# Performance work log

Hardware: AMD Instinct MI355X
Metric: run time of the kernel (lower is better)

Reference implementation:

```python
import jax, jax.numpy as jnp
import numpy as np

WINDOW_PAD = 2
OUT_NUM = 5

def setup_inputs() -> dict:
    key = jax.random.key(0)
    ks = jax.random.split(key, 7)
    B, T, E, V, H = 64, 512, 300, 50000, 2048
    in_feat = (2 * WINDOW_PAD + 1) * E + OUT_NUM * WINDOW_PAD  # 1510
    return {
        "idxs": jax.random.randint(ks[0], (B, T), 0, V),
        "emb_table": jax.random.normal(ks[1], (V, E), dtype=jnp.float32),
        "W1": jax.random.normal(ks[2], (in_feat, H), dtype=jnp.float32) * 0.02,
        "b1": jax.random.normal(ks[3], (H,), dtype=jnp.float32) * 0.02,
        "W2": jax.random.normal(ks[4], (H, OUT_NUM), dtype=jnp.float32) * 0.02,
        "b2": jax.random.normal(ks[5], (OUT_NUM,), dtype=jnp.float32) * 0.02,
        "initial_state": jnp.zeros((OUT_NUM * WINDOW_PAD,), dtype=jnp.float32),
    }

def reference(idxs, emb_table, W1, b1, W2, b2, initial_state):
    B, T = idxs.shape
    E = emb_table.shape[1]
    wp = WINDOW_PAD
    # pad token indices with 0 on both sides, gather embeddings
    idxs_pad = jnp.pad(idxs, ((0, 0), (wp, wp)))          # [B, T+2wp]
    emb_pad = emb_table[idxs_pad]                          # [B, T+2wp, E]
    # sliding windows: position t sees tokens t..t+2wp of padded seq
    win = jnp.stack([emb_pad[:, k:k + T, :] for k in range(2 * wp + 1)], axis=2)
    e = win.reshape(B, T, (2 * wp + 1) * E)                # [B, T, (2wp+1)E]
    e_t = jnp.transpose(e, (1, 0, 2))                      # [T, B, F] for scan

    prev0 = jnp.tile(initial_state[None, :], (B, 1))       # [B, out*wp]

    def step(prev, e_i):
        x_i = jnp.concatenate([e_i, prev], axis=1)         # [B, F + out*wp]
        h = jax.nn.relu(x_i @ W1 + b1)                     # [B, H]
        y_i = h @ W2 + b2                                  # [B, out]
        p = jax.nn.softmax(jax.lax.stop_gradient(y_i), axis=1)
        new_prev = jnp.concatenate([prev[:, OUT_NUM:], p], axis=1)
        return new_prev, y_i

    _, ys = jax.lax.scan(step, prev0, e_t)                 # ys: [T, B, out]
    return jnp.transpose(ys, (1, 0, 2))                    # [B, T, out]
```

## Files before the change

kernel.cpp:

```cpp
#include <hip/hip_runtime.h>

typedef __attribute__((ext_vector_type(8))) short bf16x8;
typedef __attribute__((ext_vector_type(8))) unsigned short u16x8;
typedef __attribute__((ext_vector_type(4))) float f32x4;
typedef __attribute__((ext_vector_type(2))) float f32x2;

__device__ __forceinline__ unsigned short f2bf(float f) {
  union { float f; unsigned u; } v; v.f = f;
  unsigned r = v.u + 0x7FFFu + ((v.u >> 16) & 1u);
  return (unsigned short)(r >> 16);
}
__device__ __forceinline__ float bf2f(unsigned short s) {
  union { unsigned u; float f; } v; v.u = ((unsigned)s) << 16;
  return v.f;
}
__device__ __forceinline__ float max3f(float a, float b, float c) {
  float d;
  asm("v_max3_f32 %0, %1, %2, %3" : "=v"(d) : "v"(a), "v"(b), "v"(c));
  return d;
}

template <int CTRL>
__device__ __forceinline__ float dpp_add(float v) {
  int m = __builtin_amdgcn_update_dpp(0, __float_as_int(v), CTRL, 0xf, 0xf, true);
  return v + __int_as_float(m);
}
__device__ __forceinline__ float wave_sum63(float v) {
  v = dpp_add<0x111>(v);
  v = dpp_add<0x112>(v);
  v = dpp_add<0x114>(v);
  v = dpp_add<0x118>(v);
  v = dpp_add<0x142>(v);
  v = dpp_add<0x143>(v);
  return v;
}


__global__ __launch_bounds__(256) void prep_kernel(
    const float* __restrict__ W1, unsigned short* __restrict__ W1bT,
    const int* __restrict__ idxs, const float* __restrict__ emb,
    unsigned short* __restrict__ P) {
  const int bid = blockIdx.x;
  const int tid = threadIdx.x;
  if (bid < 800) {
    __shared__ float tile[64][65];
    int kb = bid % 25;
    int hb = bid / 25;
    int win = kb / 5;
    int e0 = (kb % 5) << 6;
    int hh = tid & 63;
    int kq = tid >> 6;
#pragma unroll
    for (int kk = kq; kk < 64; kk += 4) {
      int e = e0 + kk;
      float v = 0.f;
      if (e < 300) v = W1[(size_t)(win * 300 + e) * 2048 + hb * 64 + hh];
      tile[kk][hh] = v;
    }
    __syncthreads();
    int kk = tid & 63;
    int hq = tid >> 6;
#pragma unroll
    for (int h = hq; h < 64; h += 4) {
      W1bT[(size_t)(hb * 64 + h) * 1600 + kb * 64 + kk] = f2bf(tile[kk][h]);
    }
    return;
  }
  int g4 = (bid - 800) * 4;
#pragma unroll
  for (int r = 0; r < 4; ++r) {
    int g = g4 + r;
    int b = g / 516;
    int tp = g - b * 516;
    int tok = 0;
    if (tp >= 2 && tp < 514) tok = idxs[b * 512 + tp - 2];
    const float* erow = emb + (size_t)tok * 300;
    float v = (tid < 300) ? erow[tid] : 0.f;
    P[(size_t)g * 320 + tid] = f2bf(v);
    if (tid < 64) {
      int e = tid + 256;
      float v2 = (e < 300) ? erow[e] : 0.f;
      P[(size_t)g * 320 + e] = f2bf(v2);
    }
  }
}

__global__ __launch_bounds__(256) void gemm_kernel(
    const unsigned short* __restrict__ P,
    const unsigned short* __restrict__ W1bT,
    const float* __restrict__ b1,
    unsigned short* __restrict__ Z) {
  __shared__ unsigned short smem[17408];
  unsigned short* As = smem;
  unsigned short* Bs = smem + 8192;
  const int tid = threadIdx.x;
  const int lane = tid & 63;
  const int w = tid >> 6;
  const int wm = w >> 1, wn = w & 1;
  const int lr = lane & 15;
  const int lk = (lane >> 4) << 3;

  const int nt = blockIdx.x & 15;
  const int mt = blockIdx.x >> 4;
  const int b = mt >> 2;
  const int t0 = (mt & 3) << 7;

  const unsigned short* srcA[4];
  const unsigned short* srcB[4];
#pragma unroll
  for (int j = 0; j < 4; ++j) {
    int chunk = tid + j * 256;
    int row = chunk >> 3, kb = chunk & 7;
    int kbs = kb ^ (row & 7);
    srcA[j] = P + (size_t)(b * 516 + t0 + row) * 320 + (kbs << 3);
    srcB[j] = W1bT + (size_t)(nt * 128 + row) * 1600 + (kbs << 3);
  }

  f32x4 acc[4][4];
#pragma unroll
  for (int i = 0; i < 4; i++)
#pragma unroll
    for (int j = 0; j < 4; j++) acc[i][j] = (f32x4){0.f, 0.f, 0.f, 0.f};

  for (int kt = 0; kt < 25; ++kt) {
#pragma unroll
    for (int j = 0; j < 4; ++j) {
      int chunk = tid + j * 256;
      __builtin_amdgcn_global_load_lds(
          (const __attribute__((address_space(1))) unsigned int*)srcA[j],
          (__attribute__((address_space(3))) unsigned int*)&As[chunk << 3],
          16, 0, 0);
      srcA[j] += 64;
    }
#pragma unroll
    for (int j = 0; j < 4; ++j) {
      int chunk = tid + j * 256;
      __builtin_amdgcn_global_load_lds(
          (const __attribute__((address_space(1))) unsigned int*)srcB[j],
          (__attribute__((address_space(3))) unsigned int*)&Bs[chunk << 3],
          16, 0, 0);
      srcB[j] += 64;
    }
    __syncthreads();
#pragma unroll
    for (int ks = 0; ks < 64; ks += 32) {
      const int slot = (ks + lk) >> 3;
      bf16x8 af[4], bv[4];
#pragma unroll
      for (int am = 0; am < 4; ++am) {
        int row = (wm << 6) + (am << 4) + lr;
        af[am] = *(const bf16x8*)&As[(row << 6) + ((slot ^ (row & 7)) << 3)];
      }
#pragma unroll
      for (int bn = 0; bn < 4; ++bn) {
        int col = (wn << 6) + (bn << 4) + lr;
        bv[bn] = *(const bf16x8*)&Bs[(col << 6) + ((slot ^ (col & 7)) << 3)];
      }
#pragma unroll
      for (int am = 0; am < 4; ++am)
#pragma unroll
        for (int bn = 0; bn < 4; ++bn)
          acc[am][bn] = __builtin_amdgcn_mfma_f32_16x16x32_bf16(
              af[am], bv[bn], acc[am][bn], 0, 0, 0);
    }
    __syncthreads();
  }

  {
    const int rq = lane >> 4;
    const int rloc0 = (wm << 6) + (rq << 2);
    const int cloc0 = (wn << 6) + lr;
    float b1v[4];
#pragma unroll
    for (int bn = 0; bn < 4; ++bn)
      b1v[bn] = b1[nt * 128 + cloc0 + (bn << 4)];
#pragma unroll
    for (int am = 0; am < 4; ++am)
#pragma unroll
      for (int bn = 0; bn < 4; ++bn) {
        int rl = rloc0 + (am << 4);
        int cl = cloc0 + (bn << 4);
#pragma unroll
        for (int j = 0; j < 4; ++j)
          smem[(rl + j) * 136 + cl] = f2bf(acc[am][bn][j] + b1v[bn]);
      }
    __syncthreads();
    const int chunk = tid & 15;
    const int rsub = tid >> 4;
#pragma unroll
    for (int p = 0; p < 8; ++p) {
      int row = p * 16 + rsub;
      u16x8 v = *(const u16x8*)&smem[row * 136 + chunk * 8];
      *(u16x8*)&Z[(size_t)(mt * 128 + row) * 2048 + nt * 128 + chunk * 8] = v;
    }
  }
}

__global__ __launch_bounds__(256, 1) void scan_kernel(
    const unsigned short* __restrict__ Z, const float* __restrict__ W1,
    const float* __restrict__ W2, const float* __restrict__ b2,
    const float* __restrict__ istate, float* __restrict__ out) {
  const int b = blockIdx.x;
  const int tid = threadIdx.x;
  const int lane = tid & 63;
  const int wv = tid >> 6;
  const unsigned short* Zb = Z + (size_t)b * 512 * 2048;
  float* outb = out + (size_t)b * 512 * 5;

  f32x2 w1p[4][10];
#pragma unroll
  for (int i = 0; i < 10; ++i) {
    const float* row = &W1[(size_t)(1500 + i) * 2048 + tid * 8];
#pragma unroll
    for (int q = 0; q < 4; ++q) w1p[q][i] = *(const f32x2*)&row[q * 2];
  }
  f32x2 w2p[4][5];
#pragma unroll
  for (int k = 0; k < 5; ++k)
#pragma unroll
    for (int q = 0; q < 4; ++q)
      w2p[q][k] = (f32x2){W2[(tid * 8 + 2 * q) * 5 + k],
                          W2[(tid * 8 + 2 * q + 1) * 5 + k]};
  const float b20 = b2[0], b21 = b2[1], b22 = b2[2], b23 = b2[3],
              b24 = b2[4];
  const float L2E = 1.4426950408889634f;

  __shared__ float part[2][4][8];
  __shared__ float out_lds[512][8];

  float ef0 = istate[5], ef1 = istate[6], ef2 = istate[7], ef3 = istate[8],
        ef4 = istate[9];
  float rf = 1.0f;

  u16x8 zc0 = *(const u16x8*)&Zb[tid * 8];
  u16x8 zn = *(const u16x8*)&Zb[(size_t)2048 + tid * 8];
  u16x8 zf = *(const u16x8*)&Zb[(size_t)2 * 2048 + tid * 8];
  f32x2 xc[4];
  xc[0] = (f32x2){bf2f(zc0[0]), bf2f(zc0[1])};
  xc[1] = (f32x2){bf2f(zc0[2]), bf2f(zc0[3])};
  xc[2] = (f32x2){bf2f(zc0[4]), bf2f(zc0[5])};
  xc[3] = (f32x2){bf2f(zc0[6]), bf2f(zc0[7])};
#pragma unroll
  for (int i = 0; i < 5; ++i) {
    const float oi = istate[i];
#pragma unroll
    for (int q = 0; q < 4; ++q) xc[q] = oi * w1p[q][i] + xc[q];
  }

  for (int t = 0; t < 512; ++t) {
    f32x2 sA0 = ef0 * w1p[0][5], sA1 = ef0 * w1p[1][5],
          sA2 = ef0 * w1p[2][5], sA3 = ef0 * w1p[3][5];
    sA0 = ef1 * w1p[0][6] + sA0; sA1 = ef1 * w1p[1][6] + sA1;
    sA2 = ef1 * w1p[2][6] + sA2; sA3 = ef1 * w1p[3][6] + sA3;
    sA0 = ef2 * w1p[0][7] + sA0; sA1 = ef2 * w1p[1][7] + sA1;
    sA2 = ef2 * w1p[2][7] + sA2; sA3 = ef2 * w1p[3][7] + sA3;
    sA0 = ef3 * w1p[0][8] + sA0; sA1 = ef3 * w1p[1][8] + sA1;
    sA2 = ef3 * w1p[2][8] + sA2; sA3 = ef3 * w1p[3][8] + sA3;
    sA0 = ef4 * w1p[0][9] + sA0; sA1 = ef4 * w1p[1][9] + sA1;
    sA2 = ef4 * w1p[2][9] + sA2; sA3 = ef4 * w1p[3][9] + sA3;
    f32x2 x0 = rf * sA0 + xc[0];
    f32x2 x1 = rf * sA1 + xc[1];
    f32x2 x2 = rf * sA2 + xc[2];
    f32x2 x3 = rf * sA3 + xc[3];
    const f32x2 zero2 = (f32x2){0.f, 0.f};
    x0 = __builtin_elementwise_max(x0, zero2);
    x1 = __builtin_elementwise_max(x1, zero2);
    x2 = __builtin_elementwise_max(x2, zero2);
    x3 = __builtin_elementwise_max(x3, zero2);
    f32x2 a0 = x0 * w2p[0][0] + x1 * w2p[1][0];
    f32x2 a1 = x0 * w2p[0][1] + x1 * w2p[1][1];
    f32x2 a2 = x0 * w2p[0][2] + x1 * w2p[1][2];
    f32x2 a3 = x0 * w2p[0][3] + x1 * w2p[1][3];
    f32x2 a4 = x0 * w2p[0][4] + x1 * w2p[1][4];
    a0 = x2 * w2p[2][0] + a0;  a0 = x3 * w2p[3][0] + a0;
    a1 = x2 * w2p[2][1] + a1;  a1 = x3 * w2p[3][1] + a1;
    a2 = x2 * w2p[2][2] + a2;  a2 = x3 * w2p[3][2] + a2;
    a3 = x2 * w2p[2][3] + a3;  a3 = x3 * w2p[3][3] + a3;
    a4 = x2 * w2p[2][4] + a4;  a4 = x3 * w2p[3][4] + a4;
    float y0 = a0.x + a0.y, y1 = a1.x + a1.y, y2 = a2.x + a2.y,
          y3 = a3.x + a3.y, y4 = a4.x + a4.y;

    int tn = (t + 3 < 512) ? (t + 3) : 511;
    u16x8 zfn = *(const u16x8*)&Zb[(size_t)tn * 2048 + tid * 8];

    y0 = wave_sum63(y0);
    y1 = wave_sum63(y1);
    y2 = wave_sum63(y2);
    y3 = wave_sum63(y3);
    y4 = wave_sum63(y4);
    const int pp = t & 1;
    if (lane == 63) {
      *(float4*)&part[pp][wv][0] = (float4){y0, y1, y2, y3};
      part[pp][wv][4] = y4;
    }
    asm volatile("s_waitcnt lgkmcnt(0)" ::: "memory");
    __builtin_amdgcn_sched_barrier(0);
    __builtin_amdgcn_s_barrier();
    __builtin_amdgcn_sched_barrier(0);

    f32x4 q0 = *(const f32x4*)&part[pp][0][0];
    f32x4 q1 = *(const f32x4*)&part[pp][1][0];
    f32x4 q2 = *(const f32x4*)&part[pp][2][0];
    f32x4 q3 = *(const f32x4*)&part[pp][3][0];
    f32x4 sv = (q0 + q1) + (q2 + q3);
    float s4 = (part[pp][0][4] + part[pp][1][4]) +
               (part[pp][2][4] + part[pp][3][4]);
    float s0 = sv.x + b20, s1 = sv.y + b21, s2 = sv.z + b22,
          s3 = sv.w + b23;
    s4 += b24;

    f32x2 xe0 = ef0 * w1p[0][0], xe1 = ef0 * w1p[1][0],
          xe2 = ef0 * w1p[2][0], xe3 = ef0 * w1p[3][0];
    xe0 = ef1 * w1p[0][1] + xe0; xe1 = ef1 * w1p[1][1] + xe1;
    xe2 = ef1 * w1p[2][1] + xe2; xe3 = ef1 * w1p[3][1] + xe3;
    xe0 = ef2 * w1p[0][2] + xe0; xe1 = ef2 * w1p[1][2] + xe1;
    xe2 = ef2 * w1p[2][2] + xe2; xe3 = ef2 * w1p[3][2] + xe3;
    xe0 = ef3 * w1p[0][3] + xe0; xe1 = ef3 * w1p[1][3] + xe1;
    xe2 = ef3 * w1p[2][3] + xe2; xe3 = ef3 * w1p[3][3] + xe3;
    xe0 = ef4 * w1p[0][4] + xe0; xe1 = ef4 * w1p[1][4] + xe1;
    xe2 = ef4 * w1p[2][4] + xe2; xe3 = ef4 * w1p[3][4] + xe3;
    f32x2 zn0 = (f32x2){bf2f(zn[0]), bf2f(zn[1])};
    f32x2 zn1 = (f32x2){bf2f(zn[2]), bf2f(zn[3])};
    f32x2 zn2 = (f32x2){bf2f(zn[4]), bf2f(zn[5])};
    f32x2 zn3 = (f32x2){bf2f(zn[6]), bf2f(zn[7])};
    xc[0] = rf * xe0 + zn0;
    xc[1] = rf * xe1 + zn1;
    xc[2] = rf * xe2 + zn2;
    xc[3] = rf * xe3 + zn3;

    if (tid == 0) {
      *(float4*)&out_lds[t][0] = (float4){s0, s1, s2, s3};
      out_lds[t][4] = s4;
    }

    float m = max3f(s0, s1, s2);
    m = max3f(m, s3, s4);
    float mL = m * L2E;
    ef0 = __builtin_amdgcn_exp2f(fmaf(s0, L2E, -mL));
    ef1 = __builtin_amdgcn_exp2f(fmaf(s1, L2E, -mL));
    ef2 = __builtin_amdgcn_exp2f(fmaf(s2, L2E, -mL));
    ef3 = __builtin_amdgcn_exp2f(fmaf(s3, L2E, -mL));
    ef4 = __builtin_amdgcn_exp2f(fmaf(s4, L2E, -mL));
    float d = ((ef0 + ef1) + (ef2 + ef3)) + ef4;
    rf = __builtin_amdgcn_rcpf(d);

    zn = zf; zf = zfn;
  }

  __syncthreads();
  {
    const int r0 = tid * 2, r1 = tid * 2 + 1;
    float o[10];
#pragma unroll
    for (int i = 0; i < 5; ++i) o[i] = out_lds[r0][i];
#pragma unroll
    for (int i = 0; i < 5; ++i) o[5 + i] = out_lds[r1][i];
    float* dst = outb + tid * 10;
#pragma unroll
    for (int i = 0; i < 10; ++i) dst[i] = o[i];
  }
}

extern "C" void kernel_launch(void* const* d_in, const int* in_sizes, int n_in,
                              void* d_out, int out_size, void* d_ws,
                              size_t ws_size, hipStream_t stream) {
  const int* idxs = (const int*)d_in[0];
  const float* emb = (const float*)d_in[1];
  const float* W1 = (const float*)d_in[2];
  const float* b1 = (const float*)d_in[3];
  const float* W2 = (const float*)d_in[4];
  const float* b2 = (const float*)d_in[5];
  const float* istate = (const float*)d_in[6];
  float* out = (float*)d_out;

  char* ws = (char*)d_ws;
  unsigned short* P = (unsigned short*)ws;
  unsigned short* W1bT = (unsigned short*)(ws + 21135360);
  unsigned short* Z = (unsigned short*)(ws + 21135360 + 6553600);

  hipLaunchKernelGGL(prep_kernel, dim3(800 + 8256), dim3(256), 0, stream,
                     W1, W1bT, idxs, emb, P);
  hipLaunchKernelGGL(gemm_kernel, dim3(256 * 16), dim3(256), 0, stream, P, W1bT, b1, Z);
  hipLaunchKernelGGL(scan_kernel, dim3(64), dim3(256), 0, stream, Z, W1, W2, b2,
                     istate, out);
}
```

Before: 532.6 us.

## Halve scan block to 128 threads with 16 hidden units per thread

The sequential scan kernel now uses 2 waves instead of 4, and each thread handles 16 hidden units instead of 8, so the per-step cross-wave reduction reads 2 partials instead of 4. The goal is a shorter per-timestep critical path through the barrier and LDS reduction. In exchange each thread does twice the FMA work per step and holds twice as many weights in registers, which lengthens the serial arithmetic chain and raises register pressure.

Measured after the change: 629.5 us. 1.18x slower.

```diff
diff --git a/kernel.cpp b/kernel.cpp
--- a/kernel.cpp
+++ b/kernel.cpp
@@ -196,7 +196,7 @@
   }
 }
 
-__global__ __launch_bounds__(256, 1) void scan_kernel(
+__global__ __launch_bounds__(128, 1) void scan_kernel(
     const unsigned short* __restrict__ Z, const float* __restrict__ W1,
     const float* __restrict__ W2, const float* __restrict__ b2,
     const float* __restrict__ istate, float* __restrict__ out) {
@@ -207,81 +207,80 @@
   const unsigned short* Zb = Z + (size_t)b * 512 * 2048;
   float* outb = out + (size_t)b * 512 * 5;
 
-  f32x2 w1p[4][10];
+  f32x2 w1p[8][10];
 #pragma unroll
   for (int i = 0; i < 10; ++i) {
-    const float* row = &W1[(size_t)(1500 + i) * 2048 + tid * 8];
-#pragma unroll
-    for (int q = 0; q < 4; ++q) w1p[q][i] = *(const f32x2*)&row[q * 2];
-  }
-  f32x2 w2p[4][5];
+    const float* row = &W1[(size_t)(1500 + i) * 2048 + tid * 16];
+#pragma unroll
+    for (int q = 0; q < 8; ++q) w1p[q][i] = *(const f32x2*)&row[q * 2];
+  }
+  f32x2 w2p[8][5];
 #pragma unroll
   for (int k = 0; k < 5; ++k)
 #pragma unroll
-    for (int q = 0; q < 4; ++q)
-      w2p[q][k] = (f32x2){W2[(tid * 8 + 2 * q) * 5 + k],
-                          W2[(tid * 8 + 2 * q + 1) * 5 + k]};
+    for (int q = 0; q < 8; ++q)
+      w2p[q][k] = (f32x2){W2[(tid * 16 + 2 * q) * 5 + k],
+                          W2[(tid * 16 + 2 * q + 1) * 5 + k]};
   const float b20 = b2[0], b21 = b2[1], b22 = b2[2], b23 = b2[3],
               b24 = b2[4];
   const float L2E = 1.4426950408889634f;
 
-  __shared__ float part[2][4][8];
+  __shared__ float part[2][2][8];
   __shared__ float out_lds[512][8];
 
   float ef0 = istate[5], ef1 = istate[6], ef2 = istate[7], ef3 = istate[8],
         ef4 = istate[9];
   float rf = 1.0f;
 
-  u16x8 zc0 = *(const u16x8*)&Zb[tid * 8];
-  u16x8 zn = *(const u16x8*)&Zb[(size_t)2048 + tid * 8];
-  u16x8 zf = *(const u16x8*)&Zb[(size_t)2 * 2048 + tid * 8];
-  f32x2 xc[4];
-  xc[0] = (f32x2){bf2f(zc0[0]), bf2f(zc0[1])};
-  xc[1] = (f32x2){bf2f(zc0[2]), bf2f(zc0[3])};
-  xc[2] = (f32x2){bf2f(zc0[4]), bf2f(zc0[5])};
-  xc[3] = (f32x2){bf2f(zc0[6]), bf2f(zc0[7])};
+  u16x8 zcA = *(const u16x8*)&Zb[tid * 16];
+  u16x8 zcB = *(const u16x8*)&Zb[tid * 16 + 8];
+  u16x8 znA = *(const u16x8*)&Zb[(size_t)2048 + tid * 16];
+  u16x8 znB = *(const u16x8*)&Zb[(size_t)2048 + tid * 16 + 8];
+  u16x8 zfA = *(const u16x8*)&Zb[(size_t)2 * 2048 + tid * 16];
+  u16x8 zfB = *(const u16x8*)&Zb[(size_t)2 * 2048 + tid * 16 + 8];
+
+  f32x2 xc[8];
+#pragma unroll
+  for (int q = 0; q < 4; ++q) {
+    xc[q] = (f32x2){bf2f(zcA[2 * q]), bf2f(zcA[2 * q + 1])};
+    xc[4 + q] = (f32x2){bf2f(zcB[2 * q]), bf2f(zcB[2 * q + 1])};
+  }
 #pragma unroll
   for (int i = 0; i < 5; ++i) {
     const float oi = istate[i];
 #pragma unroll
-    for (int q = 0; q < 4; ++q) xc[q] = oi * w1p[q][i] + xc[q];
+    for (int q = 0; q < 8; ++q) xc[q] = oi * w1p[q][i] + xc[q];
   }
 
   for (int t = 0; t < 512; ++t) {
-    f32x2 sA0 = ef0 * w1p[0][5], sA1 = ef0 * w1p[1][5],
-          sA2 = ef0 * w1p[2][5], sA3 = ef0 * w1p[3][5];
-    sA0 = ef1 * w1p[0][6] + sA0; sA1 = ef1 * w1p[1][6] + sA1;
-    sA2 = ef1 * w1p[2][6] + sA2; sA3 = ef1 * w1p[3][6] + sA3;
-    sA0 = ef2 * w1p[0][7] + sA0; sA1 = ef2 * w1p[1][7] + sA1;
-    sA2 = ef2 * w1p[2][7] + sA2; sA3 = ef2 * w1p[3][7] + sA3;
-    sA0 = ef3 * w1p[0][8] + sA0; sA1 = ef3 * w1p[1][8] + sA1;
-    sA2 = ef3 * w1p[2][8] + sA2; sA3 = ef3 * w1p[3][8] + sA3;
-    sA0 = ef4 * w1p[0][9] + sA0; sA1 = ef4 * w1p[1][9] + sA1;
-    sA2 = ef4 * w1p[2][9] + sA2; sA3 = ef4 * w1p[3][9] + sA3;
-    f32x2 x0 = rf * sA0 + xc[0];
-    f32x2 x1 = rf * sA1 + xc[1];
-    f32x2 x2 = rf * sA2 + xc[2];
-    f32x2 x3 = rf * sA3 + xc[3];
-    const f32x2 zero2 = (f32x2){0.f, 0.f};
-    x0 = __builtin_elementwise_max(x0, zero2);
-    x1 = __builtin_elementwise_max(x1, zero2);
-    x2 = __builtin_elementwise_max(x2, zero2);
-    x3 = __builtin_elementwise_max(x3, zero2);
-    f32x2 a0 = x0 * w2p[0][0] + x1 * w2p[1][0];
-    f32x2 a1 = x0 * w2p[0][1] + x1 * w2p[1][1];
-    f32x2 a2 = x0 * w2p[0][2] + x1 * w2p[1][2];
-    f32x2 a3 = x0 * w2p[0][3] + x1 * w2p[1][3];
-    f32x2 a4 = x0 * w2p[0][4] + x1 * w2p[1][4];
-    a0 = x2 * w2p[2][0] + a0;  a0 = x3 * w2p[3][0] + a0;
-    a1 = x2 * w2p[2][1] + a1;  a1 = x3 * w2p[3][1] + a1;
-    a2 = x2 * w2p[2][2] + a2;  a2 = x3 * w2p[3][2] + a2;
-    a3 = x2 * w2p[2][3] + a3;  a3 = x3 * w2p[3][3] + a3;
-    a4 = x2 * w2p[2][4] + a4;  a4 = x3 * w2p[3][4] + a4;
+    f32x2 x[8];
+#pragma unroll
+    for (int q = 0; q < 8; ++q) {
+      f32x2 s = ef0 * w1p[q][5];
+      s = ef1 * w1p[q][6] + s;
+      s = ef2 * w1p[q][7] + s;
+      s = ef3 * w1p[q][8] + s;
+      s = ef4 * w1p[q][9] + s;
+      x[q] = rf * s + xc[q];
+      x[q] = __builtin_elementwise_max(x[q], (f32x2){0.f, 0.f});
+    }
+    f32x2 a0 = x[0] * w2p[0][0], a1 = x[0] * w2p[0][1],
+          a2 = x[0] * w2p[0][2], a3 = x[0] * w2p[0][3],
+          a4 = x[0] * w2p[0][4];
+#pragma unroll
+    for (int q = 1; q < 8; ++q) {
+      a0 = x[q] * w2p[q][0] + a0;
+      a1 = x[q] * w2p[q][1] + a1;
+      a2 = x[q] * w2p[q][2] + a2;
+      a3 = x[q] * w2p[q][3] + a3;
+      a4 = x[q] * w2p[q][4] + a4;
+    }
     float y0 = a0.x + a0.y, y1 = a1.x + a1.y, y2 = a2.x + a2.y,
           y3 = a3.x + a3.y, y4 = a4.x + a4.y;
 
     int tn = (t + 3 < 512) ? (t + 3) : 511;
-    u16x8 zfn = *(const u16x8*)&Zb[(size_t)tn * 2048 + tid * 8];
+    u16x8 zfnA = *(const u16x8*)&Zb[(size_t)tn * 2048 + tid * 16];
+    u16x8 zfnB = *(const u16x8*)&Zb[(size_t)tn * 2048 + tid * 16 + 8];
 
     y0 = wave_sum63(y0);
     y1 = wave_sum63(y1);
@@ -300,33 +299,29 @@
 
     f32x4 q0 = *(const f32x4*)&part[pp][0][0];
     f32x4 q1 = *(const f32x4*)&part[pp][1][0];
-    f32x4 q2 = *(const f32x4*)&part[pp][2][0];
-    f32x4 q3 = *(const f32x4*)&part[pp][3][0];
-    f32x4 sv = (q0 + q1) + (q2 + q3);
-    float s4 = (part[pp][0][4] + part[pp][1][4]) +
-               (part[pp][2][4] + part[pp][3][4]);
+    f32x4 sv = q0 + q1;
+    float s4 = part[pp][0][4] + part[pp][1][4];
     float s0 = sv.x + b20, s1 = sv.y + b21, s2 = sv.z + b22,
           s3 = sv.w + b23;
     s4 += b24;
 
-    f32x2 xe0 = ef0 * w1p[0][0], xe1 = ef0 * w1p[1][0],
-          xe2 = ef0 * w1p[2][0], xe3 = ef0 * w1p[3][0];
-    xe0 = ef1 * w1p[0][1] + xe0; xe1 = ef1 * w1p[1][1] + xe1;
-    xe2 = ef1 * w1p[2][1] + xe2; xe3 = ef1 * w1p[3][1] + xe3;
-    xe0 = ef2 * w1p[0][2] + xe0; xe1 = ef2 * w1p[1][2] + xe1;
-    xe2 = ef2 * w1p[2][2] + xe2; xe3 = ef2 * w1p[3][2] + xe3;
-    xe0 = ef3 * w1p[0][3] + xe0; xe1 = ef3 * w1p[1][3] + xe1;
-    xe2 = ef3 * w1p[2][3] + xe2; xe3 = ef3 * w1p[3][3] + xe3;
-    xe0 = ef4 * w1p[0][4] + xe0; xe1 = ef4 * w1p[1][4] + xe1;
-    xe2 = ef4 * w1p[2][4] + xe2; xe3 = ef4 * w1p[3][4] + xe3;
-    f32x2 zn0 = (f32x2){bf2f(zn[0]), bf2f(zn[1])};
-    f32x2 zn1 = (f32x2){bf2f(zn[2]), bf2f(zn[3])};
-    f32x2 zn2 = (f32x2){bf2f(zn[4]), bf2f(zn[5])};
-    f32x2 zn3 = (f32x2){bf2f(zn[6]), bf2f(zn[7])};
-    xc[0] = rf * xe0 + zn0;
-    xc[1] = rf * xe1 + zn1;
-    xc[2] = rf * xe2 + zn2;
-    xc[3] = rf * xe3 + zn3;
+    f32x2 xe[8];
+#pragma unroll
+    for (int q = 0; q < 8; ++q) {
+      f32x2 s = ef0 * w1p[q][0];
+      s = ef1 * w1p[q][1] + s;
+      s = ef2 * w1p[q][2] + s;
+      s = ef3 * w1p[q][3] + s;
+      s = ef4 * w1p[q][4] + s;
+      xe[q] = s;
+    }
+#pragma unroll
+    for (int q = 0; q < 4; ++q) {
+      f32x2 za = (f32x2){bf2f(znA[2 * q]), bf2f(znA[2 * q + 1])};
+      f32x2 zb = (f32x2){bf2f(znB[2 * q]), bf2f(znB[2 * q + 1])};
+      xc[q] = rf * xe[q] + za;
+      xc[4 + q] = rf * xe[4 + q] + zb;
+    }
 
     if (tid == 0) {
       *(float4*)&out_lds[t][0] = (float4){s0, s1, s2, s3};
@@ -344,20 +339,19 @@
     float d = ((ef0 + ef1) + (ef2 + ef3)) + ef4;
     rf = __builtin_amdgcn_rcpf(d);
 
-    zn = zf; zf = zfn;
+    znA = zfA; znB = zfB;
+    zfA = zfnA; zfB = zfnB;
   }
 
   __syncthreads();
   {
-    const int r0 = tid * 2, r1 = tid * 2 + 1;
-    float o[10];
-#pragma unroll
-    for (int i = 0; i < 5; ++i) o[i] = out_lds[r0][i];
-#pragma unroll
-    for (int i = 0; i < 5; ++i) o[5 + i] = out_lds[r1][i];
-    float* dst = outb + tid * 10;
-#pragma unroll
-    for (int i = 0; i < 10; ++i) dst[i] = o[i];
+    float* dst = outb + tid * 20;
+#pragma unroll
+    for (int r = 0; r < 4; ++r) {
+      const int row = tid * 4 + r;
+#pragma unroll
+      for (int i = 0; i < 5; ++i) dst[r * 5 + i] = out_lds[row][i];
+    }
   }
 }
 
@@ -381,6 +375,6 @@
   hipLaunchKernelGGL(prep_kernel, dim3(800 + 8256), dim3(256), 0, stream,
                      W1, W1bT, idxs, emb, P);
   hipLaunchKernelGGL(gemm_kernel, dim3(256 * 16), dim3(256), 0, stream, P, W1bT, b1, Z);
-  hipLaunchKernelGGL(scan_kernel, dim3(64), dim3(256), 0, stream, Z, W1, W2, b2,
+  hipLaunchKernelGGL(scan_kernel, dim3(64), dim3(128), 0, stream, Z, W1, W2, b2,
                      istate, out);
 }
```
